# Kernel tuning notes

Hardware: AMD Instinct MI355X
Metric: run time of the kernel (lower is better)

The kernel has to match this reference:

```python
import jax, jax.numpy as jnp
import numpy as np

BS, C, D_IN, D_OUT, H = 64, 512, 256, 256, 4
HD = D_OUT // H


def setup_inputs() -> dict:
    key = jax.random.key(0)
    ks = jax.random.split(key, 8)
    def xavier(k, shape):
        fan_in, fan_out = shape[-1], shape[-2] if len(shape) > 1 else shape[-1]
        lim = float(np.sqrt(6.0 / (fan_in + fan_out)))
        return jax.random.uniform(k, shape, jnp.float32, -lim, lim)
    return {
        "h": jax.random.normal(ks[0], (BS, C, D_IN), jnp.float32),
        "A_fc": jax.random.uniform(ks[1], (BS, C, C), jnp.float32),
        "W": xavier(ks[2], (D_OUT, D_IN)),            # Linear(in_dim,out_dim,bias=False).weight
        "a": xavier(ks[3], (H, 2 * HD)),               # attention vector per head
        "W1": xavier(ks[4], (64, D_OUT)),              # channel_agg Linear(out_dim,64)
        "b1": jnp.zeros((64,), jnp.float32),
        "W2": xavier(ks[5], (1, 64)),                  # channel_agg Linear(64,1)
        "b2": jnp.zeros((1,), jnp.float32),
    }


def reference(h, A_fc, W, a, W1, b1, W2, b2):
    bs, c, _ = h.shape
    heads, hd = a.shape[0], a.shape[1] // 2
    # Wh: [BS, C, H, hd]
    Wh = (h @ W.T).reshape(bs, c, heads, hd)
    # a . cat(Wh_i, Wh_j) decomposes into two small projections broadcast-added
    e_i = jnp.einsum('nchd,hd->nch', Wh, a[:, :hd])   # varies over node i
    e_j = jnp.einsum('nchd,hd->nch', Wh, a[:, hd:])   # varies over node j
    e = e_i[:, :, None, :] + e_j[:, None, :, :]        # [BS, Ci, Cj, H]
    e = jax.nn.leaky_relu(e, negative_slope=0.2)
    e = jnp.transpose(e, (0, 3, 1, 2))                 # [BS, H, C, C]
    # prior-weighted scores, softmax over neighbors j (dropout = identity in eval)
    attn = jax.nn.softmax(e * A_fc[:, None, :, :], axis=-1)
    # aggregate: [BS,H,C,C] @ [BS,H,C,hd] -> [BS,C,H,hd] -> [BS,C,out_dim]
    h_prime = jnp.einsum('nhij,njhd->nihd', attn, Wh).reshape(bs, c, heads * hd)
    # channel gating MLP + softmax over channel dim
    s = jnp.tanh(h_prime @ W1.T + b1) @ W2.T + b2      # [BS, C, 1]
    w = jax.nn.softmax(s, axis=1)
    return jnp.sum(h_prime * w, axis=1)                # [BS, out_dim]
```

## Files before the change

### kernel.cpp

```cpp
#include <hip/hip_runtime.h>
#include <hip/hip_bf16.h>

#define BS 64
#define C 512
#define DIN 256
#define DOUT 256
#define H 4
#define HD 64

typedef __attribute__((ext_vector_type(8))) short short8;
typedef __attribute__((ext_vector_type(4))) short short4v;
typedef __attribute__((ext_vector_type(4))) float f32x4;

__device__ __forceinline__ short bfc(float f) {
    union { __hip_bfloat16 h; unsigned short s; } u;
    u.h = __float2bfloat16(f);
    return (short)u.s;
}

__device__ __forceinline__ float bf2f(short v) {
    union { unsigned u; float f; } x;
    x.u = ((unsigned)(unsigned short)v) << 16;
    return x.f;
}

__device__ __forceinline__ short8 pack8n(const float* p) {
    short8 r;
#pragma unroll
    for (int i = 0; i < 8; ++i) r[i] = bfc(p[i]);
    return r;
}

__global__ __launch_bounds__(256) void k0_prep(
    const float* __restrict__ W, const float* __restrict__ W1,
    short* __restrict__ Wbf, short* __restrict__ W1bf)
{
    const int idx = blockIdx.x * 256 + threadIdx.x;
    if (idx < 8192) {
        float t[8];
        *(float4*)(t)     = *(const float4*)(W + idx * 8);
        *(float4*)(t + 4) = *(const float4*)(W + idx * 8 + 4);
        *(short8*)(Wbf + idx * 8) = pack8n(t);
    } else if (idx < 10240) {
        const int j = idx - 8192;
        float t[8];
        *(float4*)(t)     = *(const float4*)(W1 + j * 8);
        *(float4*)(t + 4) = *(const float4*)(W1 + j * 8 + 4);
        *(short8*)(W1bf + j * 8) = pack8n(t);
    }
}

__global__ __launch_bounds__(256) void k1_gemm(
    const float* __restrict__ hsrc, const short* __restrict__ Wbf,
    const float* __restrict__ avec,
    short* __restrict__ whT, float* __restrict__ ei, float* __restrict__ ej)
{
    __shared__ __align__(16) short hs[64 * 256];
    const int tid = threadIdx.x;
    const int l = tid & 63;
    const int w = tid >> 6;
    const int lr = l & 15;
    const int g = l >> 4;
    const int kg = g * 8;
    const int mtile = blockIdx.x;
    const int row0 = mtile * 64;
    const float L2E = 1.44269504088896f;

#pragma unroll
    for (int it = 0; it < 8; ++it) {
        const int idx = tid + it * 256;
        const int row = idx >> 5;
        const int colg = idx & 31;
        const float* p = hsrc + (size_t)(row0 + row) * DIN + colg * 8;
        float t[8];
        *(float4*)(t)     = *(const float4*)(p);
        *(float4*)(t + 4) = *(const float4*)(p + 4);
        const int off = (row * 512 + colg * 16) ^ ((row & 7) << 4);
        *(short8*)((char*)hs + off) = pack8n(t);
    }
    __syncthreads();

    const int head = w;
    f32x4 acc[4][4];
#pragma unroll
    for (int i = 0; i < 4; ++i)
#pragma unroll
        for (int j = 0; j < 4; ++j) acc[i][j] = f32x4{0.f, 0.f, 0.f, 0.f};

    for (int k0 = 0; k0 < DIN; k0 += 32) {
        short8 af[4];
#pragma unroll
        for (int rt = 0; rt < 4; ++rt) {
            const int row = rt * 16 + lr;
            const int off = (row * 512 + (k0 + kg) * 2) ^ ((row & 7) << 4);
            af[rt] = *(const short8*)((const char*)hs + off);
        }
        short8 bfr[4];
#pragma unroll
        for (int ct = 0; ct < 4; ++ct)
            bfr[ct] = *(const short8*)(Wbf + (size_t)(head * 64 + ct * 16 + lr) * DIN + k0 + kg);
#pragma unroll
        for (int rt = 0; rt < 4; ++rt)
#pragma unroll
            for (int ct = 0; ct < 4; ++ct)
                acc[rt][ct] = __builtin_amdgcn_mfma_f32_16x16x32_bf16(
                    af[rt], bfr[ct], acc[rt][ct], 0, 0, 0);
    }

    float avi[4], avj[4];
#pragma unroll
    for (int ct = 0; ct < 4; ++ct) {
        avi[ct] = avec[head * 2 * HD + ct * 16 + lr];
        avj[ct] = avec[head * 2 * HD + HD + ct * 16 + lr];
    }

    const int jt = mtile & 7;
    const int bb = mtile >> 3;
    short* fragb = whT + (size_t)(bb * H + head) * (HD * C);

#pragma unroll
    for (int rt = 0; rt < 4; ++rt) {
        const int lane2 = lr + 16 * ((rt & 1) * 2 + (g >> 1));
        const int t0 = (g & 1) * 4;
        const int half = rt >> 1;
#pragma unroll
        for (int ct = 0; ct < 4; ++ct) {
            short4v sv;
#pragma unroll
            for (int reg = 0; reg < 4; ++reg) sv[reg] = bfc(acc[rt][ct][reg]);
            *(short4v*)(fragb + (jt * 4 + ct) * 1024 + half * 512 + lane2 * 8 + t0) = sv;
        }
#pragma unroll
        for (int reg = 0; reg < 4; ++reg) {
            const int j = row0 + rt * 16 + g * 4 + reg;
            const int b = j >> 9;
            const int c = j & 511;
            float pi = 0.f, pj = 0.f;
#pragma unroll
            for (int ct = 0; ct < 4; ++ct) {
                pi += acc[rt][ct][reg] * avi[ct];
                pj += acc[rt][ct][reg] * avj[ct];
            }
#pragma unroll
            for (int off = 1; off < 16; off <<= 1) {
                pi += __shfl_xor(pi, off);
                pj += __shfl_xor(pj, off);
            }
            if (lr == 0) {
                ei[(b * H + head) * C + c] = pi * L2E;
                ej[(b * H + head) * C + c] = pj * L2E;
            }
        }
    }
}

__global__ __launch_bounds__(256) void k2_attn(
    const float* __restrict__ Afc, const short* __restrict__ whT,
    const float* __restrict__ ei, const float* __restrict__ ej,
    short* __restrict__ hpb)
{
    __shared__ __align__(16) short alds[16 * 520];
    __shared__ __align__(16) float elds[4 * 512];
    const int tid = threadIdx.x;
    const int l = tid & 63;
    const int hh = tid >> 6;
    const int swz = (blockIdx.x & 7) * 256 + (blockIdx.x >> 3);
    const int b = swz >> 5;
    const int i0 = (swz & 31) * 16;
    const int lr = l & 15;
    const int kg = (l >> 4) * 8;

    {
        const float* asrc = Afc + ((size_t)b * C + i0) * C;
#pragma unroll
        for (int k = 0; k < 4; ++k) {
            const int idx = tid + k * 256;
            const int row = idx >> 6;
            const int colg = idx & 63;
            const float* p = asrc + row * 512 + colg * 8;
            float t[8];
            *(float4*)(t)     = *(const float4*)(p);
            *(float4*)(t + 4) = *(const float4*)(p + 4);
            *(short8*)(alds + row * 520 + colg * 8) = pack8n(t);
        }
        const float* ejsrc = ej + (size_t)b * H * C;
#pragma unroll
        for (int k = 0; k < 2; ++k) {
            const int idx = tid + k * 256;
            *(float4*)(elds + idx * 4) = *(const float4*)(ejsrc + idx * 4);
        }
    }
    __syncthreads();

    f32x4 O[4];
#pragma unroll
    for (int dt = 0; dt < 4; ++dt) O[dt] = f32x4{0.f, 0.f, 0.f, 0.f};
    float ls0 = 0.f, ls1 = 0.f, ls2 = 0.f, ls3 = 0.f;

    const float eiv = ei[(b * H + hh) * C + i0 + lr];
    const short* vb = whT + (size_t)(b * H + hh) * (HD * C);
    const short* arowp = alds + lr * 520;
    const float* ejl = elds + hh * 512;

    for (int jt = 0; jt < 8; ++jt) {
        const int j0 = jt * 64;

        short8 vf[4][2];
#pragma unroll
        for (int dt = 0; dt < 4; ++dt) {
            const short* vp = vb + (jt * 4 + dt) * 1024 + l * 8;
            vf[dt][0] = *(const short8*)(vp);
            vf[dt][1] = *(const short8*)(vp + 512);
        }

        float ejv[16];
        *(float4*)(ejv)      = *(const float4*)(ejl + j0 + kg);
        *(float4*)(ejv + 4)  = *(const float4*)(ejl + j0 + kg + 4);
        *(float4*)(ejv + 8)  = *(const float4*)(ejl + j0 + 32 + kg);
        *(float4*)(ejv + 12) = *(const float4*)(ejl + j0 + 32 + kg + 4);

        union { short8 s; unsigned u[4]; } a0, a1;
        a0.s = *(const short8*)(arowp + j0 + kg);
        a1.s = *(const short8*)(arowp + j0 + 32 + kg);
        float av[16];
#pragma unroll
        for (int i = 0; i < 4; ++i) {
            union { unsigned u; float f; } lo, hi;
            lo.u = a0.u[i] << 16;
            hi.u = a0.u[i] & 0xffff0000u;
            av[2 * i]     = lo.f;
            av[2 * i + 1] = hi.f;
            lo.u = a1.u[i] << 16;
            hi.u = a1.u[i] & 0xffff0000u;
            av[8 + 2 * i]     = lo.f;
            av[8 + 2 * i + 1] = hi.f;
        }

#pragma unroll
        for (int t = 0; t < 16; ++t) {
            const float z = eiv + ejv[t];
            const float zl = fmaxf(z, 0.2f * z);
            av[t] = exp2f(zl * av[t]);
        }

        union { short8 s; unsigned u[4]; } P0, P1;
#pragma unroll
        for (int i = 0; i < 4; ++i) {
            const unsigned b0 = __float_as_uint(av[2 * i])     & 0xffff0000u;
            const unsigned b1 = __float_as_uint(av[2 * i + 1]) & 0xffff0000u;
            ls0 += __uint_as_float(b0);
            ls1 += __uint_as_float(b1);
            P0.u[i] = (b0 >> 16) | b1;
            const unsigned c0 = __float_as_uint(av[8 + 2 * i])     & 0xffff0000u;
            const unsigned c1 = __float_as_uint(av[8 + 2 * i + 1]) & 0xffff0000u;
            ls2 += __uint_as_float(c0);
            ls3 += __uint_as_float(c1);
            P1.u[i] = (c0 >> 16) | c1;
        }

#pragma unroll
        for (int dt = 0; dt < 4; ++dt) {
            O[dt] = __builtin_amdgcn_mfma_f32_16x16x32_bf16(P0.s, vf[dt][0], O[dt], 0, 0, 0);
            O[dt] = __builtin_amdgcn_mfma_f32_16x16x32_bf16(P1.s, vf[dt][1], O[dt], 0, 0, 0);
        }
    }

    float lsum = (ls0 + ls1) + (ls2 + ls3);
    lsum += __shfl_xor(lsum, 16);
    lsum += __shfl_xor(lsum, 32);
    const float inv = 1.0f / lsum;
    float fr[4];
#pragma unroll
    for (int reg = 0; reg < 4; ++reg)
        fr[reg] = __shfl(inv, (l >> 4) * 4 + reg);
#pragma unroll
    for (int dt = 0; dt < 4; ++dt)
#pragma unroll
        for (int reg = 0; reg < 4; ++reg) {
            const int c = i0 + (l >> 4) * 4 + reg;
            hpb[((size_t)b * C + c) * DOUT + hh * HD + dt * 16 + lr] =
                bfc(O[dt][reg] * fr[reg]);
        }
}

__global__ __launch_bounds__(256) void k3_gate(
    const short* __restrict__ hpb, const short* __restrict__ W1bf,
    const float* __restrict__ b1, const float* __restrict__ W2,
    const float* __restrict__ b2, float* __restrict__ sgate)
{
    __shared__ __align__(16) short hs[64 * 256];
    const int t = threadIdx.x;
    const int l = t & 63;
    const int w = t >> 6;
    const int b = blockIdx.x >> 3;
    const int c0 = (blockIdx.x & 7) * 64;
    const int lr = l & 15;
    const int kg = (l >> 4) * 8;

    {
        const short* src = hpb + ((size_t)b * C + c0) * DOUT;
#pragma unroll
        for (int it = 0; it < 8; ++it) {
            const int idx = t + it * 256;
            const int row = idx >> 5;
            const int colg = idx & 31;
            const int off = (row * 512 + colg * 16) ^ ((row & 7) << 4);
            *(short8*)((char*)hs + off) = *(const short8*)(src + row * 256 + colg * 8);
        }
    }
    __syncthreads();

    f32x4 acc[4];
#pragma unroll
    for (int ct = 0; ct < 4; ++ct) acc[ct] = f32x4{0.f, 0.f, 0.f, 0.f};

    const int myrow = w * 16 + lr;
    for (int k0 = 0; k0 < DOUT; k0 += 32) {
        const int off = (myrow * 512 + (k0 + kg) * 2) ^ ((myrow & 7) << 4);
        const short8 af = *(const short8*)((const char*)hs + off);
#pragma unroll
        for (int ct = 0; ct < 4; ++ct) {
            const short8 bfr = *(const short8*)(W1bf + (size_t)(ct * 16 + lr) * DOUT + k0 + kg);
            acc[ct] = __builtin_amdgcn_mfma_f32_16x16x32_bf16(af, bfr, acc[ct], 0, 0, 0);
        }
    }

    float b1v[4], w2v[4];
#pragma unroll
    for (int ct = 0; ct < 4; ++ct) {
        b1v[ct] = b1[ct * 16 + lr];
        w2v[ct] = W2[ct * 16 + lr];
    }
    const float b2v = b2[0];
#pragma unroll
    for (int reg = 0; reg < 4; ++reg) {
        float val = 0.f;
#pragma unroll
        for (int ct = 0; ct < 4; ++ct)
            val += tanhf(acc[ct][reg] + b1v[ct]) * w2v[ct];
#pragma unroll
        for (int off = 1; off < 16; off <<= 1) val += __shfl_xor(val, off);
        if (lr == 0)
            sgate[b * C + c0 + w * 16 + (l >> 4) * 4 + reg] = val + b2v;
    }
}

__global__ __launch_bounds__(256) void k4a_partial(
    const short* __restrict__ hpb, const float* __restrict__ sgate,
    float* __restrict__ partial)
{
    __shared__ float red[16];
    __shared__ float wlds[64];
    const int t = threadIdx.x;
    const int b = blockIdx.x >> 3;
    const int c0 = (blockIdx.x & 7) * 64;
    const int l = t & 63, w = t >> 6;
    const float L2E = 1.44269504088896f;

    const float s0 = sgate[b * C + t], s1 = sgate[b * C + 256 + t];
    float mx = fmaxf(s0, s1);
#pragma unroll
    for (int off = 1; off < 64; off <<= 1) mx = fmaxf(mx, __shfl_xor(mx, off));
    if (l == 0) red[w] = mx;
    __syncthreads();
    mx = fmaxf(fmaxf(red[0], red[1]), fmaxf(red[2], red[3]));
    float sum = exp2f((s0 - mx) * L2E) + exp2f((s1 - mx) * L2E);
#pragma unroll
    for (int off = 1; off < 64; off <<= 1) sum += __shfl_xor(sum, off);
    if (l == 0) red[8 + w] = sum;
    __syncthreads();
    sum = red[8] + red[9] + red[10] + red[11];
    const float inv = 1.f / sum;
    if (t < 64)
        wlds[t] = exp2f((sgate[b * C + c0 + t] - mx) * L2E) * inv;
    __syncthreads();

    float acc = 0.f;
    const short* base = hpb + ((size_t)b * C + c0) * DOUT + t;
#pragma unroll 4
    for (int c = 0; c < 64; ++c) acc += wlds[c] * bf2f(base[(size_t)c * DOUT]);
    partial[(size_t)blockIdx.x * DOUT + t] = acc;
}

__global__ __launch_bounds__(256) void k4b_reduce(
    const float* __restrict__ partial, float* __restrict__ out)
{
    const int t = threadIdx.x;
    const int b = blockIdx.x;
    float s = 0.f;
#pragma unroll
    for (int k = 0; k < 8; ++k)
        s += partial[(size_t)(b * 8 + k) * DOUT + t];
    out[b * DOUT + t] = s;
}

extern "C" void kernel_launch(void* const* d_in, const int* in_sizes, int n_in,
                              void* d_out, int out_size, void* d_ws, size_t ws_size,
                              hipStream_t stream) {
    const float* hsrc = (const float*)d_in[0];
    const float* Afc  = (const float*)d_in[1];
    const float* W    = (const float*)d_in[2];
    const float* avec = (const float*)d_in[3];
    const float* W1   = (const float*)d_in[4];
    const float* b1   = (const float*)d_in[5];
    const float* W2   = (const float*)d_in[6];
    const float* b2   = (const float*)d_in[7];

    char* ws = (char*)d_ws;
    short* whT   = (short*)(ws);
    float* ei    = (float*)(ws + 16777216);
    float* ej    = (float*)(ws + 17301504);
    short* hpb   = (short*)(ws + 17825792);
    float* sg    = (float*)(ws + 34603008);
    float* parts = (float*)(ws + 34734080);
    short* Wbf   = (short*)(ws + 35258368);
    short* W1bf  = (short*)(ws + 35389440);

    hipLaunchKernelGGL(k0_prep, dim3(40), dim3(256), 0, stream, W, W1, Wbf, W1bf);
    hipLaunchKernelGGL(k1_gemm, dim3(512), dim3(256), 0, stream, hsrc, Wbf, avec, whT, ei, ej);
    hipLaunchKernelGGL(k2_attn, dim3(2048), dim3(256), 0, stream, Afc, whT, ei, ej, hpb);
    hipLaunchKernelGGL(k3_gate, dim3(512), dim3(256), 0, stream, hpb, W1bf, b1, W2, b2, sg);
    hipLaunchKernelGGL(k4a_partial, dim3(512), dim3(256), 0, stream, hpb, sg, parts);
    hipLaunchKernelGGL(k4b_reduce, dim3(64), dim3(256), 0, stream, parts, (float*)d_out);
}
```

Baseline: 82.19 us.

## Fuse final weighted-sum kernels and use native exp2 in attention

Merges the partial-sum and reduce kernels into one 1024-thread block per batch. Each block computes the channel softmax once and reduces four 128-channel strips through shared memory, which removes a launch and the global partial buffer. The attention kernel now uses the native exp2 builtin and advances a single V pointer per tile instead of recomputing the address. The final stage runs only 64 blocks, so it uses fewer CUs than the previous 512-block partial kernel.

```diff
diff --git a/kernel.cpp b/kernel.cpp
--- a/kernel.cpp
+++ b/kernel.cpp
@@ -198,7 +198,7 @@
     float ls0 = 0.f, ls1 = 0.f, ls2 = 0.f, ls3 = 0.f;
 
     const float eiv = ei[(b * H + hh) * C + i0 + lr];
-    const short* vb = whT + (size_t)(b * H + hh) * (HD * C);
+    const short* vpw = whT + (size_t)(b * H + hh) * (HD * C) + l * 8;
     const short* arowp = alds + lr * 520;
     const float* ejl = elds + hh * 512;
 
@@ -208,9 +208,8 @@
         short8 vf[4][2];
 #pragma unroll
         for (int dt = 0; dt < 4; ++dt) {
-            const short* vp = vb + (jt * 4 + dt) * 1024 + l * 8;
-            vf[dt][0] = *(const short8*)(vp);
-            vf[dt][1] = *(const short8*)(vp + 512);
+            vf[dt][0] = *(const short8*)(vpw + dt * 1024);
+            vf[dt][1] = *(const short8*)(vpw + dt * 1024 + 512);
         }
 
         float ejv[16];
@@ -240,7 +239,7 @@
         for (int t = 0; t < 16; ++t) {
             const float z = eiv + ejv[t];
             const float zl = fmaxf(z, 0.2f * z);
-            av[t] = exp2f(zl * av[t]);
+            av[t] = __builtin_amdgcn_exp2f(zl * av[t]);
         }
 
         union { short8 s; unsigned u[4]; } P0, P1;
@@ -263,6 +262,7 @@
             O[dt] = __builtin_amdgcn_mfma_f32_16x16x32_bf16(P0.s, vf[dt][0], O[dt], 0, 0, 0);
             O[dt] = __builtin_amdgcn_mfma_f32_16x16x32_bf16(P1.s, vf[dt][1], O[dt], 0, 0, 0);
         }
+        vpw += 4096;
     }
 
     float lsum = (ls0 + ls1) + (ls2 + ls3);
@@ -345,53 +345,61 @@
     }
 }
 
-__global__ __launch_bounds__(256) void k4a_partial(
+__global__ __launch_bounds__(1024) void k4_out(
     const short* __restrict__ hpb, const float* __restrict__ sgate,
-    float* __restrict__ partial)
+    float* __restrict__ out)
 {
-    __shared__ float red[16];
-    __shared__ float wlds[64];
+    __shared__ float wlds[512];
+    __shared__ float red[32];
+    __shared__ float partial[4][256];
     const int t = threadIdx.x;
-    const int b = blockIdx.x >> 3;
-    const int c0 = (blockIdx.x & 7) * 64;
+    const int b = blockIdx.x;
     const int l = t & 63, w = t >> 6;
     const float L2E = 1.44269504088896f;
 
-    const float s0 = sgate[b * C + t], s1 = sgate[b * C + 256 + t];
-    float mx = fmaxf(s0, s1);
+    float s = (t < 512) ? sgate[b * C + t] : -1e30f;
+    float mx = s;
 #pragma unroll
     for (int off = 1; off < 64; off <<= 1) mx = fmaxf(mx, __shfl_xor(mx, off));
     if (l == 0) red[w] = mx;
     __syncthreads();
-    mx = fmaxf(fmaxf(red[0], red[1]), fmaxf(red[2], red[3]));
-    float sum = exp2f((s0 - mx) * L2E) + exp2f((s1 - mx) * L2E);
+    if (t < 32) {
+        float m = (t < 16) ? red[t] : -1e30f;
+#pragma unroll
+        for (int off = 1; off < 16; off <<= 1) m = fmaxf(m, __shfl_xor(m, off));
+        if (t == 0) red[0] = m;
+    }
+    __syncthreads();
+    mx = red[0];
+
+    float e = (t < 512) ? __builtin_amdgcn_exp2f((s - mx) * L2E) : 0.f;
+    float sum = e;
 #pragma unroll
     for (int off = 1; off < 64; off <<= 1) sum += __shfl_xor(sum, off);
-    if (l == 0) red[8 + w] = sum;
-    __syncthreads();
-    sum = red[8] + red[9] + red[10] + red[11];
-    const float inv = 1.f / sum;
-    if (t < 64)
-        wlds[t] = exp2f((sgate[b * C + c0 + t] - mx) * L2E) * inv;
-    __syncthreads();
-
+    if (l == 0) red[16 + w] = sum;
+    __syncthreads();
+    if (t < 32) {
+        float m = (t < 16) ? red[16 + t] : 0.f;
+#pragma unroll
+        for (int off = 1; off < 16; off <<= 1) m += __shfl_xor(m, off);
+        if (t == 0) red[16] = m;
+    }
+    __syncthreads();
+    const float inv = 1.f / red[16];
+    if (t < 512) wlds[t] = e * inv;
+    __syncthreads();
+
+    const int strip = t >> 8;
+    const int d = t & 255;
     float acc = 0.f;
-    const short* base = hpb + ((size_t)b * C + c0) * DOUT + t;
+    const short* base = hpb + ((size_t)b * C + strip * 128) * DOUT + d;
+    const float* wp = wlds + strip * 128;
 #pragma unroll 4
-    for (int c = 0; c < 64; ++c) acc += wlds[c] * bf2f(base[(size_t)c * DOUT]);
-    partial[(size_t)blockIdx.x * DOUT + t] = acc;
-}
-
-__global__ __launch_bounds__(256) void k4b_reduce(
-    const float* __restrict__ partial, float* __restrict__ out)
-{
-    const int t = threadIdx.x;
-    const int b = blockIdx.x;
-    float s = 0.f;
-#pragma unroll
-    for (int k = 0; k < 8; ++k)
-        s += partial[(size_t)(b * 8 + k) * DOUT + t];
-    out[b * DOUT + t] = s;
+    for (int c = 0; c < 128; ++c) acc += wp[c] * bf2f(base[(size_t)c * DOUT]);
+    partial[strip][d] = acc;
+    __syncthreads();
+    if (t < 256)
+        out[b * DOUT + t] = (partial[0][t] + partial[1][t]) + (partial[2][t] + partial[3][t]);
 }
 
 extern "C" void kernel_launch(void* const* d_in, const int* in_sizes, int n_in,
@@ -412,14 +420,12 @@
     float* ej    = (float*)(ws + 17301504);
     short* hpb   = (short*)(ws + 17825792);
     float* sg    = (float*)(ws + 34603008);
-    float* parts = (float*)(ws + 34734080);
-    short* Wbf   = (short*)(ws + 35258368);
-    short* W1bf  = (short*)(ws + 35389440);
+    short* Wbf   = (short*)(ws + 34734080);
+    short* W1bf  = (short*)(ws + 34865152);
 
     hipLaunchKernelGGL(k0_prep, dim3(40), dim3(256), 0, stream, W, W1, Wbf, W1bf);
     hipLaunchKernelGGL(k1_gemm, dim3(512), dim3(256), 0, stream, hsrc, Wbf, avec, whT, ei, ej);
     hipLaunchKernelGGL(k2_attn, dim3(2048), dim3(256), 0, stream, Afc, whT, ei, ej, hpb);
     hipLaunchKernelGGL(k3_gate, dim3(512), dim3(256), 0, stream, hpb, W1bf, b1, W2, b2, sg);
-    hipLaunchKernelGGL(k4a_partial, dim3(512), dim3(256), 0, stream, hpb, sg, parts);
-    hipLaunchKernelGGL(k4b_reduce, dim3(64), dim3(256), 0, stream, parts, (float*)d_out);
-}
+    hipLaunchKernelGGL(k4_out, dim3(64), dim3(1024), 0, stream, hpb, sg, (float*)d_out);
+}
```

New measurement: 81.76 us. About the same (-0.5%).
